# Kernel tuning notes

Hardware: AMD Instinct MI355X
Metric: run time of the kernel (lower is better)

Reference implementation:

```python
import jax, jax.numpy as jnp
import numpy as np

F_FIELDS = 39
VOCAB = 100000
EMB = 16
BATCH = 16384
H1, H2 = 32, 32


def setup_inputs() -> dict:
    key = jax.random.key(0)
    ks = jax.random.split(key, 10)
    Xi = jax.random.randint(ks[0], (BATCH, F_FIELDS, 1), 0, VOCAB, dtype=jnp.int64 if jax.config.jax_enable_x64 else jnp.int32).astype(jnp.int32)
    Xv = jax.random.uniform(ks[1], (BATCH, F_FIELDS), dtype=jnp.float32)
    # per-field embedding tables, stacked (all feature_sizes equal)
    emb1 = jax.random.normal(ks[2], (F_FIELDS, VOCAB, 1), dtype=jnp.float32)
    emb2 = jax.random.normal(ks[3], (F_FIELDS, VOCAB, EMB), dtype=jnp.float32)
    d_in = F_FIELDS * EMB
    W1 = jax.random.normal(ks[4], (d_in, H1), dtype=jnp.float32) / np.sqrt(d_in)
    b1 = jnp.zeros((H1,), dtype=jnp.float32)
    W2 = jax.random.normal(ks[5], (H1, H2), dtype=jnp.float32) / np.sqrt(H1)
    b2 = jnp.zeros((H2,), dtype=jnp.float32)
    bias = jax.random.normal(ks[6], (1,), dtype=jnp.float32)
    return {"Xi": Xi, "Xv": Xv, "emb1": emb1, "emb2": emb2,
            "W1": W1, "b1": b1, "W2": W2, "b2": b2, "bias": bias}


def reference(Xi, Xv, emb1, emb2, W1, b1, W2, b2, bias):
    B = Xi.shape[0]
    idx = Xi[:, :, 0]  # [B, F]
    # flatten per-field tables into one big table; offset indices by field
    off = idx + (jnp.arange(F_FIELDS, dtype=idx.dtype) * VOCAB)[None, :]  # [B, F]
    # first order: gather scalar per (b, f), scale by Xv
    first = emb1.reshape(F_FIELDS * VOCAB)[off] * Xv  # [B, F]
    # second order embeddings, scaled by Xv
    e2 = emb2.reshape(F_FIELDS * VOCAB, EMB)[off] * Xv[:, :, None]  # [B, F, E]
    s = jnp.sum(e2, axis=1)                      # [B, E]
    sq_sum = jnp.sum(e2 * e2, axis=1)            # [B, E]
    fm_second = 0.5 * (s * s - sq_sum)           # [B, E]
    # deep part on concatenated field embeddings
    deep_in = e2.reshape(B, F_FIELDS * EMB)
    h = jax.nn.relu(deep_in @ W1 + b1)
    h = jax.nn.relu(h @ W2 + b2)
    total = jnp.sum(first, axis=1) + jnp.sum(fm_second, axis=1) + jnp.sum(h, axis=1) + bias
    return total  # [B]
```

## Files before the change

kernel.cpp:

```cpp
#include <hip/hip_runtime.h>
#include <hip/hip_bf16.h>

#define F_FIELDS 39
#define VOCAB    100000
#define EMB      16
#define BATCH    16384
#define H1       32
#define H2       32
#define KSTEPS   20
#define KPW      5

typedef __bf16 bf16x8 __attribute__((ext_vector_type(8)));
typedef float  f32x4  __attribute__((ext_vector_type(4)));

__global__ __launch_bounds__(256) void swizzle_w1_kernel(const float* __restrict__ W1,
                                                         __bf16* __restrict__ ws)
{
    int fidx = blockIdx.x * 256 + threadIdx.x;
    if (fidx >= KSTEPS * 2 * 64) return;
    int lane = fidx & 63;
    int nh   = (fidx >> 6) & 1;
    int ks   = fidx >> 7;
    int k0   = ks * 32 + (lane >> 4) * 8;
    int n    = nh * 16 + (lane & 15);
    __bf16 vals[8];
    #pragma unroll
    for (int j = 0; j < 8; ++j) {
        int k = k0 + j;
        vals[j] = (k < F_FIELDS * EMB) ? (__bf16)W1[k * H1 + n] : (__bf16)0.0f;
    }
    *reinterpret_cast<bf16x8*>(&ws[fidx * 8]) = *reinterpret_cast<const bf16x8*>(vals);
}

__global__ __launch_bounds__(256, 4) void deepfm_main(
    const int*   __restrict__ Xi,  const float* __restrict__ Xv,
    const float* __restrict__ emb1,const float* __restrict__ emb2,
    const __bf16* __restrict__ wsW1,
    const float* __restrict__ b1,  const float* __restrict__ W2,
    const float* __restrict__ b2,  const float* __restrict__ bias,
    float* __restrict__ out)
{
    __shared__ int   sXi[16 * F_FIELDS];
    __shared__ float sXv[16 * F_FIELDS];
    __shared__ float pacc[4][16][32];
    __shared__ float sbuf[4][16][16];
    __shared__ float qbuf[4][16];
    __shared__ float fbuf[4][16];
    __shared__ float W2s[H1 * H2];
    __shared__ float hs[16][32];

    const int t    = threadIdx.x;
    const int h    = t >> 6;
    const int l    = t & 63;
    const int sloc = l & 15;
    const int q    = l >> 4;
    const int fpar = q >> 1;
    const int eoff = (q & 1) * 8;
    const int blk  = blockIdx.x;

    {
        const int base = blk * 16 * F_FIELDS;
        #pragma unroll
        for (int i = t; i < 16 * F_FIELDS; i += 256) {
            sXi[i] = Xi[base + i];
            sXv[i] = Xv[base + i];
        }
    }
    reinterpret_cast<float4*>(W2s)[t] = reinterpret_cast<const float4*>(W2)[t];
    __syncthreads();

    float xvm[KPW];
    float4 g0[KPW], g1[KPW];
    #pragma unroll
    for (int ks = 0; ks < KPW; ++ks) {
        int f = 8 * ks + 2 * h + fpar;
        bool v = (f < F_FIELDS);
        int fi = v ? f : 0;
        int idx = sXi[sloc * F_FIELDS + fi];
        xvm[ks] = v ? sXv[sloc * F_FIELDS + fi] : 0.0f;
        const float4* rp = reinterpret_cast<const float4*>(emb2 + (fi * VOCAB + idx) * EMB + eoff);
        g0[ks] = rp[0];
        g1[ks] = rp[1];
    }
    float e1v[3]; float xvf[3];
    #pragma unroll
    for (int i = 0; i < 3; ++i) {
        int f = 4 * h + q + 16 * i;
        bool v = (f < F_FIELDS);
        int fi = v ? f : 0;
        int idx = sXi[sloc * F_FIELDS + fi];
        xvf[i] = v ? sXv[sloc * F_FIELDS + fi] : 0.0f;
        e1v[i] = emb1[fi * VOCAB + idx];
    }

    const bf16x8* wsf = reinterpret_cast<const bf16x8*>(wsW1);
    f32x4 acc0 = {0.f,0.f,0.f,0.f}, acc1 = {0.f,0.f,0.f,0.f};
    float sa[8];
    float qq = 0.f;
    #pragma unroll
    for (int j = 0; j < 8; ++j) sa[j] = 0.f;

    #pragma unroll
    for (int ks = 0; ks < KPW; ++ks) {
        int kstep = 4 * ks + h;
        bf16x8 fr0 = wsf[(kstep * 2 + 0) * 64 + l];
        bf16x8 fr1 = wsf[(kstep * 2 + 1) * 64 + l];
        float xv = xvm[ks];
        float e[8] = { g0[ks].x*xv, g0[ks].y*xv, g0[ks].z*xv, g0[ks].w*xv,
                       g1[ks].x*xv, g1[ks].y*xv, g1[ks].z*xv, g1[ks].w*xv };
        bf16x8 a;
        #pragma unroll
        for (int j = 0; j < 8; ++j) {
            a[j] = (__bf16)e[j];
            sa[j] += e[j];
            qq   += e[j]*e[j];
        }
        acc0 = __builtin_amdgcn_mfma_f32_16x16x32_bf16(a, fr0, acc0, 0, 0, 0);
        acc1 = __builtin_amdgcn_mfma_f32_16x16x32_bf16(a, fr1, acc1, 0, 0, 0);
    }

    float sf[8];
    #pragma unroll
    for (int j = 0; j < 8; ++j) sf[j] = sa[j] + __shfl_xor(sa[j], 32);
    qq += __shfl_xor(qq, 32);
    qq += __shfl_xor(qq, 16);
    if (q < 2) {
        float4* srow = reinterpret_cast<float4*>(&sbuf[h][sloc][q * 8]);
        srow[0] = make_float4(sf[0], sf[1], sf[2], sf[3]);
        srow[1] = make_float4(sf[4], sf[5], sf[6], sf[7]);
    }
    if (l < 16) qbuf[h][sloc] = qq;

    float facc = 0.f;
    #pragma unroll
    for (int i = 0; i < 3; ++i) facc += e1v[i] * xvf[i];
    facc += __shfl_xor(facc, 16);
    facc += __shfl_xor(facc, 32);
    if (l < 16) fbuf[h][sloc] = facc;

    float badd0 = (h == 0) ? b1[sloc]      : 0.f;
    float badd1 = (h == 0) ? b1[16 + sloc] : 0.f;
    #pragma unroll
    for (int r = 0; r < 4; ++r) {
        int row = q * 4 + r;
        pacc[h][row][sloc]      = acc0[r] + badd0;
        pacc[h][row][16 + sloc] = acc1[r] + badd1;
    }
    __syncthreads();

    {
        int s = t >> 4, c = t & 15;
        hs[s][c]      = fmaxf(pacc[0][s][c]      + pacc[1][s][c]      + pacc[2][s][c]      + pacc[3][s][c],      0.f);
        hs[s][c + 16] = fmaxf(pacc[0][s][c + 16] + pacc[1][s][c + 16] + pacc[2][s][c + 16] + pacc[3][s][c + 16], 0.f);
    }
    __syncthreads();

    const int s = t >> 4;
    const int u = t & 15;

    float sv = sbuf[0][s][u] + sbuf[1][s][u] + sbuf[2][s][u] + sbuf[3][s][u];
    float s2 = sv * sv;

    float a0 = b2[2 * u], a1 = b2[2 * u + 1];
    #pragma unroll
    for (int i = 0; i < H1; ++i) {
        float hv = hs[s][i];
        a0 += hv * W2s[i * H2 + 2 * u];
        a1 += hv * W2s[i * H2 + 2 * u + 1];
    }
    float psum = fmaxf(a0, 0.f) + fmaxf(a1, 0.f);

    psum += __shfl_xor(psum, 1);  s2 += __shfl_xor(s2, 1);
    psum += __shfl_xor(psum, 2);  s2 += __shfl_xor(s2, 2);
    psum += __shfl_xor(psum, 4);  s2 += __shfl_xor(s2, 4);
    psum += __shfl_xor(psum, 8);  s2 += __shfl_xor(s2, 8);

    if (u == 0) {
        float qtot = qbuf[0][s] + qbuf[1][s] + qbuf[2][s] + qbuf[3][s];
        float ftot = fbuf[0][s] + fbuf[1][s] + fbuf[2][s] + fbuf[3][s];
        out[blk * 16 + s] = psum + 0.5f * (s2 - qtot) + ftot + bias[0];
    }
}

extern "C" void kernel_launch(void* const* d_in, const int* in_sizes, int n_in,
                              void* d_out, int out_size, void* d_ws, size_t ws_size,
                              hipStream_t stream) {
    const int*   Xi   = (const int*)  d_in[0];
    const float* Xv   = (const float*)d_in[1];
    const float* emb1 = (const float*)d_in[2];
    const float* emb2 = (const float*)d_in[3];
    const float* W1   = (const float*)d_in[4];
    const float* b1   = (const float*)d_in[5];
    const float* W2   = (const float*)d_in[6];
    const float* b2   = (const float*)d_in[7];
    const float* bias = (const float*)d_in[8];
    float* out = (float*)d_out;
    __bf16* ws = (__bf16*)d_ws;

    swizzle_w1_kernel<<<(KSTEPS*2*64 + 255)/256, 256, 0, stream>>>(W1, ws);
    deepfm_main<<<BATCH/16, 256, 0, stream>>>(Xi, Xv, emb1, emb2, ws, b1, W2, b2, bias, out);
}
```

Measured before the change: 34.62 us.

## Stage bf16 embeddings through LDS with 16-byte nontemporal gathers per lane

Changes the gather pattern so each lane loads one 16-byte quarter of an embedding row, which means four lanes cover one 64-byte row, and uses nontemporal loads. The scaled values are written as bf16 into a shared-memory tile, and after a barrier the MFMA A-fragments are read back from that tile. The goal is more memory-level parallelism, with more independent small loads in flight, and keeping random embedding rows from polluting the cache. In exchange it adds about 20KB of LDS, an extra barrier and an LDS round trip, which may reduce occupancy.

```diff
diff --git a/kernel.cpp b/kernel.cpp
--- a/kernel.cpp
+++ b/kernel.cpp
@@ -9,8 +9,10 @@
 #define H2       32
 #define KSTEPS   20
 #define KPW      5
+#define GPW      10
 
 typedef __bf16 bf16x8 __attribute__((ext_vector_type(8)));
+typedef __bf16 bf16x4 __attribute__((ext_vector_type(4)));
 typedef float  f32x4  __attribute__((ext_vector_type(4)));
 
 __global__ __launch_bounds__(256) void swizzle_w1_kernel(const float* __restrict__ W1,
@@ -42,6 +44,7 @@
 {
     __shared__ int   sXi[16 * F_FIELDS];
     __shared__ float sXv[16 * F_FIELDS];
+    __shared__ __align__(16) __bf16 eds[40][16][16];
     __shared__ float pacc[4][16][32];
     __shared__ float sbuf[4][16][16];
     __shared__ float qbuf[4][16];
@@ -52,15 +55,12 @@
     const int t    = threadIdx.x;
     const int h    = t >> 6;
     const int l    = t & 63;
-    const int sloc = l & 15;
+    const int s    = l & 15;
     const int q    = l >> 4;
-    const int fpar = q >> 1;
-    const int eoff = (q & 1) * 8;
     const int blk  = blockIdx.x;
 
     {
         const int base = blk * 16 * F_FIELDS;
-        #pragma unroll
         for (int i = t; i < 16 * F_FIELDS; i += 256) {
             sXi[i] = Xi[base + i];
             sXv[i] = Xv[base + i];
@@ -69,102 +69,96 @@
     reinterpret_cast<float4*>(W2s)[t] = reinterpret_cast<const float4*>(W2)[t];
     __syncthreads();
 
-    float xvm[KPW];
-    float4 g0[KPW], g1[KPW];
+    f32x4 g[GPW]; float xvg[GPW];
     #pragma unroll
-    for (int ks = 0; ks < KPW; ++ks) {
-        int f = 8 * ks + 2 * h + fpar;
+    for (int i = 0; i < GPW; ++i) {
+        int f  = h + 4 * i;
         bool v = (f < F_FIELDS);
         int fi = v ? f : 0;
-        int idx = sXi[sloc * F_FIELDS + fi];
-        xvm[ks] = v ? sXv[sloc * F_FIELDS + fi] : 0.0f;
-        const float4* rp = reinterpret_cast<const float4*>(emb2 + (fi * VOCAB + idx) * EMB + eoff);
-        g0[ks] = rp[0];
-        g1[ks] = rp[1];
+        int idx = sXi[s * F_FIELDS + fi];
+        xvg[i]  = v ? sXv[s * F_FIELDS + fi] : 0.0f;
+        const f32x4* rp = reinterpret_cast<const f32x4*>(emb2 + (fi * VOCAB + idx) * EMB) + q;
+        g[i] = __builtin_nontemporal_load(rp);
     }
-    float e1v[3]; float xvf[3];
+    float e1v[3], xvf[3];
     #pragma unroll
     for (int i = 0; i < 3; ++i) {
-        int f = 4 * h + q + 16 * i;
+        int f  = 4 * h + q + 16 * i;
         bool v = (f < F_FIELDS);
         int fi = v ? f : 0;
-        int idx = sXi[sloc * F_FIELDS + fi];
-        xvf[i] = v ? sXv[sloc * F_FIELDS + fi] : 0.0f;
-        e1v[i] = emb1[fi * VOCAB + idx];
+        int idx = sXi[s * F_FIELDS + fi];
+        xvf[i] = v ? sXv[s * F_FIELDS + fi] : 0.0f;
+        e1v[i] = __builtin_nontemporal_load(emb1 + (fi * VOCAB + idx));
     }
 
-    const bf16x8* wsf = reinterpret_cast<const bf16x8*>(wsW1);
-    f32x4 acc0 = {0.f,0.f,0.f,0.f}, acc1 = {0.f,0.f,0.f,0.f};
-    float sa[8];
+    float sa4[4] = {0.f, 0.f, 0.f, 0.f};
     float qq = 0.f;
     #pragma unroll
-    for (int j = 0; j < 8; ++j) sa[j] = 0.f;
-
-    #pragma unroll
-    for (int ks = 0; ks < KPW; ++ks) {
-        int kstep = 4 * ks + h;
-        bf16x8 fr0 = wsf[(kstep * 2 + 0) * 64 + l];
-        bf16x8 fr1 = wsf[(kstep * 2 + 1) * 64 + l];
-        float xv = xvm[ks];
-        float e[8] = { g0[ks].x*xv, g0[ks].y*xv, g0[ks].z*xv, g0[ks].w*xv,
-                       g1[ks].x*xv, g1[ks].y*xv, g1[ks].z*xv, g1[ks].w*xv };
-        bf16x8 a;
-        #pragma unroll
-        for (int j = 0; j < 8; ++j) {
-            a[j] = (__bf16)e[j];
-            sa[j] += e[j];
-            qq   += e[j]*e[j];
-        }
-        acc0 = __builtin_amdgcn_mfma_f32_16x16x32_bf16(a, fr0, acc0, 0, 0, 0);
-        acc1 = __builtin_amdgcn_mfma_f32_16x16x32_bf16(a, fr1, acc1, 0, 0, 0);
+    for (int i = 0; i < GPW; ++i) {
+        int f = h + 4 * i;
+        float xv = xvg[i];
+        float e0 = g[i][0] * xv, e1 = g[i][1] * xv, e2 = g[i][2] * xv, e3 = g[i][3] * xv;
+        sa4[0] += e0; sa4[1] += e1; sa4[2] += e2; sa4[3] += e3;
+        qq += e0*e0 + e1*e1 + e2*e2 + e3*e3;
+        bf16x4 bv = { (__bf16)e0, (__bf16)e1, (__bf16)e2, (__bf16)e3 };
+        *reinterpret_cast<bf16x4*>(&eds[f][s][q * 4]) = bv;
     }
 
-    float sf[8];
-    #pragma unroll
-    for (int j = 0; j < 8; ++j) sf[j] = sa[j] + __shfl_xor(sa[j], 32);
+    *reinterpret_cast<float4*>(&sbuf[h][s][q * 4]) = make_float4(sa4[0], sa4[1], sa4[2], sa4[3]);
+    qq += __shfl_xor(qq, 16);
     qq += __shfl_xor(qq, 32);
-    qq += __shfl_xor(qq, 16);
-    if (q < 2) {
-        float4* srow = reinterpret_cast<float4*>(&sbuf[h][sloc][q * 8]);
-        srow[0] = make_float4(sf[0], sf[1], sf[2], sf[3]);
-        srow[1] = make_float4(sf[4], sf[5], sf[6], sf[7]);
-    }
-    if (l < 16) qbuf[h][sloc] = qq;
+    if (l < 16) qbuf[h][s] = qq;
 
     float facc = 0.f;
     #pragma unroll
     for (int i = 0; i < 3; ++i) facc += e1v[i] * xvf[i];
     facc += __shfl_xor(facc, 16);
     facc += __shfl_xor(facc, 32);
-    if (l < 16) fbuf[h][sloc] = facc;
+    if (l < 16) fbuf[h][s] = facc;
 
-    float badd0 = (h == 0) ? b1[sloc]      : 0.f;
-    float badd1 = (h == 0) ? b1[16 + sloc] : 0.f;
+    __syncthreads();
+
+    const bf16x8* wsf = reinterpret_cast<const bf16x8*>(wsW1);
+    f32x4 acc0 = {0.f,0.f,0.f,0.f}, acc1 = {0.f,0.f,0.f,0.f};
+    #pragma unroll
+    for (int j = 0; j < KPW; ++j) {
+        int ks = h + 4 * j;
+        int f  = 2 * ks + (q >> 1);
+        int p0 = (q & 1) * 8;
+        bf16x8 afr = *reinterpret_cast<const bf16x8*>(&eds[f][s][p0]);
+        bf16x8 b0  = wsf[(ks * 2 + 0) * 64 + l];
+        bf16x8 b1f = wsf[(ks * 2 + 1) * 64 + l];
+        acc0 = __builtin_amdgcn_mfma_f32_16x16x32_bf16(afr, b0,  acc0, 0, 0, 0);
+        acc1 = __builtin_amdgcn_mfma_f32_16x16x32_bf16(afr, b1f, acc1, 0, 0, 0);
+    }
+
+    float badd0 = (h == 0) ? b1[s]      : 0.f;
+    float badd1 = (h == 0) ? b1[16 + s] : 0.f;
     #pragma unroll
     for (int r = 0; r < 4; ++r) {
         int row = q * 4 + r;
-        pacc[h][row][sloc]      = acc0[r] + badd0;
-        pacc[h][row][16 + sloc] = acc1[r] + badd1;
+        pacc[h][row][s]      = acc0[r] + badd0;
+        pacc[h][row][16 + s] = acc1[r] + badd1;
     }
     __syncthreads();
 
     {
-        int s = t >> 4, c = t & 15;
-        hs[s][c]      = fmaxf(pacc[0][s][c]      + pacc[1][s][c]      + pacc[2][s][c]      + pacc[3][s][c],      0.f);
-        hs[s][c + 16] = fmaxf(pacc[0][s][c + 16] + pacc[1][s][c + 16] + pacc[2][s][c + 16] + pacc[3][s][c + 16], 0.f);
+        int ss = t >> 4, c = t & 15;
+        hs[ss][c]      = fmaxf(pacc[0][ss][c]      + pacc[1][ss][c]      + pacc[2][ss][c]      + pacc[3][ss][c],      0.f);
+        hs[ss][c + 16] = fmaxf(pacc[0][ss][c + 16] + pacc[1][ss][c + 16] + pacc[2][ss][c + 16] + pacc[3][ss][c + 16], 0.f);
     }
     __syncthreads();
 
-    const int s = t >> 4;
-    const int u = t & 15;
+    const int so = t >> 4;
+    const int u  = t & 15;
 
-    float sv = sbuf[0][s][u] + sbuf[1][s][u] + sbuf[2][s][u] + sbuf[3][s][u];
+    float sv = sbuf[0][so][u] + sbuf[1][so][u] + sbuf[2][so][u] + sbuf[3][so][u];
     float s2 = sv * sv;
 
     float a0 = b2[2 * u], a1 = b2[2 * u + 1];
     #pragma unroll
     for (int i = 0; i < H1; ++i) {
-        float hv = hs[s][i];
+        float hv = hs[so][i];
         a0 += hv * W2s[i * H2 + 2 * u];
         a1 += hv * W2s[i * H2 + 2 * u + 1];
     }
@@ -176,9 +170,9 @@
     psum += __shfl_xor(psum, 8);  s2 += __shfl_xor(s2, 8);
 
     if (u == 0) {
-        float qtot = qbuf[0][s] + qbuf[1][s] + qbuf[2][s] + qbuf[3][s];
-        float ftot = fbuf[0][s] + fbuf[1][s] + fbuf[2][s] + fbuf[3][s];
-        out[blk * 16 + s] = psum + 0.5f * (s2 - qtot) + ftot + bias[0];
+        float qtot = qbuf[0][so] + qbuf[1][so] + qbuf[2][so] + qbuf[3][so];
+        float ftot = fbuf[0][so] + fbuf[1][so] + fbuf[2][so] + fbuf[3][so];
+        out[blk * 16 + so] = psum + 0.5f * (s2 - qtot) + ftot + bias[0];
     }
 }
 
```

New measurement: 39.09 us. 1.13x slower.

## Move first-order embedding gather into a separate field-major prep kernel

Applied to the files above, without the earlier changes.

The first-order emb1 gather-and-scale moves out of the main kernel into a prep kernel. That kernel walks one field per block group, so neighbouring gathers hit the same per-field table, and it writes the scaled values to a workspace buffer. The main kernel then sums 39 contiguous floats per sample instead of doing scattered gathers and shuffle reductions. This lowers register and latency pressure in the main kernel, at the cost of an extra workspace round trip and a larger prep launch that reads Xi and Xv one more time.

```diff
diff --git a/kernel.cpp b/kernel.cpp
--- a/kernel.cpp
+++ b/kernel.cpp
@@ -9,33 +9,51 @@
 #define H2       32
 #define KSTEPS   20
 #define KPW      5
+#define FRAG_OFF (640*1024)
 
 typedef __bf16 bf16x8 __attribute__((ext_vector_type(8)));
 typedef float  f32x4  __attribute__((ext_vector_type(4)));
 
-__global__ __launch_bounds__(256) void swizzle_w1_kernel(const float* __restrict__ W1,
-                                                         __bf16* __restrict__ ws)
+__global__ __launch_bounds__(256) void prep_kernel(
+    const int*   __restrict__ Xi,  const float* __restrict__ Xv,
+    const float* __restrict__ emb1,const float* __restrict__ W1,
+    float* __restrict__ ws1, __bf16* __restrict__ wsfrag)
 {
-    int fidx = blockIdx.x * 256 + threadIdx.x;
-    if (fidx >= KSTEPS * 2 * 64) return;
-    int lane = fidx & 63;
-    int nh   = (fidx >> 6) & 1;
-    int ks   = fidx >> 7;
-    int k0   = ks * 32 + (lane >> 4) * 8;
-    int n    = nh * 16 + (lane & 15);
-    __bf16 vals[8];
-    #pragma unroll
-    for (int j = 0; j < 8; ++j) {
-        int k = k0 + j;
-        vals[j] = (k < F_FIELDS * EMB) ? (__bf16)W1[k * H1 + n] : (__bf16)0.0f;
-    }
-    *reinterpret_cast<bf16x8*>(&ws[fidx * 8]) = *reinterpret_cast<const bf16x8*>(vals);
+    const int blk = blockIdx.x;
+    const int fld   = blk >> 5;
+    const int chunk = blk & 31;
+    const int t = threadIdx.x;
+    const int b0 = chunk * 512 + t * 2;
+    #pragma unroll
+    for (int j = 0; j < 2; ++j) {
+        int b = b0 + j;
+        int idx  = Xi[b * F_FIELDS + fld];
+        float xv = Xv[b * F_FIELDS + fld];
+        ws1[b * F_FIELDS + fld] = emb1[fld * VOCAB + idx] * xv;
+    }
+    if (blk < 10) {
+        int fidx = blk * 256 + t;
+        if (fidx < KSTEPS * 2 * 64) {
+            int lane = fidx & 63;
+            int nh   = (fidx >> 6) & 1;
+            int ks   = fidx >> 7;
+            int k0   = ks * 32 + (lane >> 4) * 8;
+            int n    = nh * 16 + (lane & 15);
+            __bf16 vals[8];
+            #pragma unroll
+            for (int j = 0; j < 8; ++j) {
+                int k = k0 + j;
+                vals[j] = (k < F_FIELDS * EMB) ? (__bf16)W1[k * H1 + n] : (__bf16)0.0f;
+            }
+            *reinterpret_cast<bf16x8*>(&wsfrag[fidx * 8]) = *reinterpret_cast<const bf16x8*>(vals);
+        }
+    }
 }
 
 __global__ __launch_bounds__(256, 4) void deepfm_main(
     const int*   __restrict__ Xi,  const float* __restrict__ Xv,
-    const float* __restrict__ emb1,const float* __restrict__ emb2,
-    const __bf16* __restrict__ wsW1,
+    const float* __restrict__ emb2,
+    const __bf16* __restrict__ wsW1, const float* __restrict__ ws1,
     const float* __restrict__ b1,  const float* __restrict__ W2,
     const float* __restrict__ b2,  const float* __restrict__ bias,
     float* __restrict__ out)
@@ -45,7 +63,6 @@
     __shared__ float pacc[4][16][32];
     __shared__ float sbuf[4][16][16];
     __shared__ float qbuf[4][16];
-    __shared__ float fbuf[4][16];
     __shared__ float W2s[H1 * H2];
     __shared__ float hs[16][32];
 
@@ -60,7 +77,6 @@
 
     {
         const int base = blk * 16 * F_FIELDS;
-        #pragma unroll
         for (int i = t; i < 16 * F_FIELDS; i += 256) {
             sXi[i] = Xi[base + i];
             sXv[i] = Xv[base + i];
@@ -81,16 +97,6 @@
         const float4* rp = reinterpret_cast<const float4*>(emb2 + (fi * VOCAB + idx) * EMB + eoff);
         g0[ks] = rp[0];
         g1[ks] = rp[1];
-    }
-    float e1v[3]; float xvf[3];
-    #pragma unroll
-    for (int i = 0; i < 3; ++i) {
-        int f = 4 * h + q + 16 * i;
-        bool v = (f < F_FIELDS);
-        int fi = v ? f : 0;
-        int idx = sXi[sloc * F_FIELDS + fi];
-        xvf[i] = v ? sXv[sloc * F_FIELDS + fi] : 0.0f;
-        e1v[i] = emb1[fi * VOCAB + idx];
     }
 
     const bf16x8* wsf = reinterpret_cast<const bf16x8*>(wsW1);
@@ -131,13 +137,6 @@
     }
     if (l < 16) qbuf[h][sloc] = qq;
 
-    float facc = 0.f;
-    #pragma unroll
-    for (int i = 0; i < 3; ++i) facc += e1v[i] * xvf[i];
-    facc += __shfl_xor(facc, 16);
-    facc += __shfl_xor(facc, 32);
-    if (l < 16) fbuf[h][sloc] = facc;
-
     float badd0 = (h == 0) ? b1[sloc]      : 0.f;
     float badd1 = (h == 0) ? b1[16 + sloc] : 0.f;
     #pragma unroll
@@ -149,26 +148,30 @@
     __syncthreads();
 
     {
-        int s = t >> 4, c = t & 15;
-        hs[s][c]      = fmaxf(pacc[0][s][c]      + pacc[1][s][c]      + pacc[2][s][c]      + pacc[3][s][c],      0.f);
-        hs[s][c + 16] = fmaxf(pacc[0][s][c + 16] + pacc[1][s][c + 16] + pacc[2][s][c + 16] + pacc[3][s][c + 16], 0.f);
+        int ss = t >> 4, c = t & 15;
+        hs[ss][c]      = fmaxf(pacc[0][ss][c]      + pacc[1][ss][c]      + pacc[2][ss][c]      + pacc[3][ss][c],      0.f);
+        hs[ss][c + 16] = fmaxf(pacc[0][ss][c + 16] + pacc[1][ss][c + 16] + pacc[2][ss][c + 16] + pacc[3][ss][c + 16], 0.f);
     }
     __syncthreads();
 
-    const int s = t >> 4;
-    const int u = t & 15;
-
-    float sv = sbuf[0][s][u] + sbuf[1][s][u] + sbuf[2][s][u] + sbuf[3][s][u];
+    const int so = t >> 4;
+    const int u  = t & 15;
+
+    float sv = sbuf[0][so][u] + sbuf[1][so][u] + sbuf[2][so][u] + sbuf[3][so][u];
     float s2 = sv * sv;
 
+    const float* w1row = ws1 + (blk * 16 + so) * F_FIELDS;
+    float fo = w1row[u] + w1row[16 + u];
+    if (u < 7) fo += w1row[32 + u];
+
     float a0 = b2[2 * u], a1 = b2[2 * u + 1];
     #pragma unroll
     for (int i = 0; i < H1; ++i) {
-        float hv = hs[s][i];
+        float hv = hs[so][i];
         a0 += hv * W2s[i * H2 + 2 * u];
         a1 += hv * W2s[i * H2 + 2 * u + 1];
     }
-    float psum = fmaxf(a0, 0.f) + fmaxf(a1, 0.f);
+    float psum = fmaxf(a0, 0.f) + fmaxf(a1, 0.f) + fo;
 
     psum += __shfl_xor(psum, 1);  s2 += __shfl_xor(s2, 1);
     psum += __shfl_xor(psum, 2);  s2 += __shfl_xor(s2, 2);
@@ -176,9 +179,8 @@
     psum += __shfl_xor(psum, 8);  s2 += __shfl_xor(s2, 8);
 
     if (u == 0) {
-        float qtot = qbuf[0][s] + qbuf[1][s] + qbuf[2][s] + qbuf[3][s];
-        float ftot = fbuf[0][s] + fbuf[1][s] + fbuf[2][s] + fbuf[3][s];
-        out[blk * 16 + s] = psum + 0.5f * (s2 - qtot) + ftot + bias[0];
+        float qtot = qbuf[0][so] + qbuf[1][so] + qbuf[2][so] + qbuf[3][so];
+        out[blk * 16 + so] = psum + 0.5f * (s2 - qtot) + bias[0];
     }
 }
 
@@ -195,8 +197,10 @@
     const float* b2   = (const float*)d_in[7];
     const float* bias = (const float*)d_in[8];
     float* out = (float*)d_out;
-    __bf16* ws = (__bf16*)d_ws;
-
-    swizzle_w1_kernel<<<(KSTEPS*2*64 + 255)/256, 256, 0, stream>>>(W1, ws);
-    deepfm_main<<<BATCH/16, 256, 0, stream>>>(Xi, Xv, emb1, emb2, ws, b1, W2, b2, bias, out);
+
+    float*  ws1    = (float*)d_ws;
+    __bf16* wsfrag = (__bf16*)((float*)d_ws + FRAG_OFF);
+
+    prep_kernel<<<F_FIELDS * 32, 256, 0, stream>>>(Xi, Xv, emb1, W1, ws1, wsfrag);
+    deepfm_main<<<BATCH/16, 256, 0, stream>>>(Xi, Xv, emb2, wsfrag, ws1, b1, W2, b2, bias, out);
 }
```

Measured after the change: 36.05 us. +4.1%, slower.
